# Kernel optimization log

Measured on AMD Instinct MI355X. Metric: run time of the kernel, lower is better.

Reference implementation:

```python
import jax, jax.numpy as jnp
import numpy as np

TEMPERATURE = 0.1
LOSS_SCALE = 1.0
LAMBD = 0.5


def setup_inputs() -> dict:
    key = jax.random.key(0)
    k1, k2 = jax.random.split(key)
    B, D = 4096, 768
    predicted = jax.random.normal(k1, (B, D), dtype=jnp.float32)
    target = jax.random.normal(k2, (B, D), dtype=jnp.float32)
    return {"predicted": predicted, "target": target}


def reference(predicted, target):
    predicted = predicted.astype(jnp.float32)
    target = target.astype(jnp.float32)
    B = predicted.shape[0]

    # Pairwise L2 distances via Gram identity (avoids B x B x D intermediate):
    # ||p_i - t_j||^2 = ||p_i||^2 + ||t_j||^2 - 2 p_i . t_j
    p_sq = jnp.sum(predicted * predicted, axis=-1)  # [B]
    t_sq = jnp.sum(target * target, axis=-1)        # [B]
    cross = predicted @ target.T                    # [B, B]
    sq_dist = p_sq[:, None] + t_sq[None, :] - 2.0 * cross
    distances = jnp.sqrt(jnp.maximum(sq_dist, 0.0))  # [B, B]

    logits = -distances / TEMPERATURE
    # cross-entropy with labels = arange(B): mean of -log_softmax diagonal
    log_probs = jax.nn.log_softmax(logits, axis=-1)
    contrastive_dist_loss = -jnp.mean(jnp.diagonal(log_probs))

    # normalized L1 magnitude loss
    elementwise_l1 = jnp.sum(jnp.abs(predicted - target), axis=-1)  # [B]
    target_magnitude = jnp.sum(jnp.abs(target), axis=-1)            # [B]
    norm_factor = jax.lax.stop_gradient(target_magnitude)
    normalized_magnitude_loss = jnp.mean(elementwise_l1 / norm_factor)

    total_loss = LOSS_SCALE * (
        LAMBD * contrastive_dist_loss + (1.0 - LAMBD) * normalized_magnitude_loss
    )
    return (total_loss, contrastive_dist_loss, normalized_magnitude_loss)
```

## Files before the change

kernel.cpp:

```cpp
#include <hip/hip_runtime.h>
#include <hip/hip_bf16.h>
#include <math.h>

#define B_ROWS 4096
#define D_DIM  768

#define BM 256
#define BN 256
#define BK 32
#define NKT (D_DIM / BK)
#define NBUF 4

typedef __attribute__((ext_vector_type(8))) short bf16x8;
typedef __attribute__((ext_vector_type(4))) float f32x4;

__device__ __forceinline__ unsigned short f32_to_bf16(float x) {
    unsigned int u = __float_as_uint(x);
    return (unsigned short)((u + 0x7fffu + ((u >> 16) & 1u)) >> 16);
}

__device__ __forceinline__ void async_copy16(const unsigned short* g, unsigned short* l) {
    __builtin_amdgcn_global_load_lds(
        (const __attribute__((address_space(1))) unsigned int*)g,
        (__attribute__((address_space(3))) unsigned int*)l,
        16, 0, 0);
}

__global__ void __launch_bounds__(256) rowstats_kernel(
    const float* __restrict__ P, const float* __restrict__ T,
    unsigned short* __restrict__ Pb, unsigned short* __restrict__ Tb,
    float* __restrict__ p_sq, float* __restrict__ t_sq,
    float* __restrict__ diagl, float* __restrict__ magr,
    float* __restrict__ rowsum)
{
    const int wave = threadIdx.x >> 6, lane = threadIdx.x & 63;
    const int i = blockIdx.x * 4 + wave;
    const f32x4* prow = (const f32x4*)(P + (size_t)i * D_DIM);
    const f32x4* trow = (const f32x4*)(T + (size_t)i * D_DIM);
    ushort4* pbrow = (ushort4*)(Pb + (size_t)i * D_DIM);
    ushort4* tbrow = (ushort4*)(Tb + (size_t)i * D_DIM);

    float psq = 0.f, tsq = 0.f, cr = 0.f, l1 = 0.f, tm = 0.f;
    #pragma unroll
    for (int u = 0; u < 3; ++u) {
        const int c4 = u * 64 + lane;
        f32x4 p = prow[c4], t = trow[c4];
        #pragma unroll
        for (int k = 0; k < 4; ++k) {
            psq += p[k] * p[k]; tsq += t[k] * t[k]; cr += p[k] * t[k];
            l1 += fabsf(p[k] - t[k]); tm += fabsf(t[k]);
        }
        pbrow[c4] = make_ushort4(f32_to_bf16(p[0]), f32_to_bf16(p[1]),
                                 f32_to_bf16(p[2]), f32_to_bf16(p[3]));
        tbrow[c4] = make_ushort4(f32_to_bf16(t[0]), f32_to_bf16(t[1]),
                                 f32_to_bf16(t[2]), f32_to_bf16(t[3]));
    }
    #pragma unroll
    for (int m = 1; m < 64; m <<= 1) {
        psq += __shfl_xor(psq, m, 64);
        tsq += __shfl_xor(tsq, m, 64);
        cr  += __shfl_xor(cr,  m, 64);
        l1  += __shfl_xor(l1,  m, 64);
        tm  += __shfl_xor(tm,  m, 64);
    }
    if (lane == 0) {
        p_sq[i] = psq;
        t_sq[i] = tsq;
        float sq = fmaxf(psq + tsq - 2.0f * cr, 0.0f);
        diagl[i] = -sqrtf(sq) * 10.0f;
        magr[i]  = l1 / tm;
        rowsum[i] = 0.0f;
    }
}

__global__ void __launch_bounds__(512, 2) lse_gemm_kernel(
    const unsigned short* __restrict__ Pb, const unsigned short* __restrict__ Tb,
    const float* __restrict__ p_sq, const float* __restrict__ t_sq,
    const float* __restrict__ diagl, float* __restrict__ rowsum)
{
    __shared__ __align__(16) unsigned short S[NBUF][2][BM * BK];

    const int tid  = threadIdx.x;
    const int lane = tid & 63, wave = tid >> 6;

    const int flat = blockIdx.x;
    const int xcd  = flat & 7;
    const int s    = flat >> 3;
    const int ti   = ((xcd >> 1) << 2) + (s >> 3);
    const int tj   = ((xcd & 1) << 3) + (s & 7);
    const int i0   = ti * BM, j0 = tj * BN;

    const int wm = wave >> 2, wn = wave & 3;
    const int row16 = lane & 15, quad = lane >> 4;

    int aoff[8], boff[4];
    #pragma unroll
    for (int mt = 0; mt < 8; ++mt) {
        const int R = wm * 128 + mt * 16 + row16;
        aoff[mt] = R * BK + ((quad ^ ((R >> 1) & 3)) << 3);
    }
    #pragma unroll
    for (int nt = 0; nt < 4; ++nt) {
        const int R = wn * 64 + nt * 16 + row16;
        boff[nt] = R * BK + ((quad ^ ((R >> 1) & 3)) << 3);
    }

    const bool isB = wave >= 4;
    const int  sw  = wave & 3;
    const int  q   = lane & 3;
    const unsigned short* gsrc = isB ? Tb : Pb;
    const int  r0g = isB ? j0 : i0;
    const unsigned short* gp[4];
    int lbase[4];
    #pragma unroll
    for (int j = 0; j < 4; ++j) {
        const int R = sw * 64 + j * 16 + (lane >> 2);
        const int g = q ^ ((R >> 1) & 3);
        gp[j] = gsrc + (size_t)(r0g + R) * D_DIM + g * 8;
        lbase[j] = (sw * 64 + j * 16) * BK;
    }

    f32x4 acc[8][4];
    #pragma unroll
    for (int a = 0; a < 8; ++a)
        #pragma unroll
        for (int b = 0; b < 4; ++b)
            acc[a][b] = (f32x4){0.f, 0.f, 0.f, 0.f};

    auto compute = [&](int buf) {
        const unsigned short* Ab = &S[buf][0][0];
        const unsigned short* Bb = &S[buf][1][0];
        bf16x8 a[8], b[4];
        #pragma unroll
        for (int mt = 0; mt < 8; ++mt) a[mt] = *(const bf16x8*)(Ab + aoff[mt]);
        #pragma unroll
        for (int nt = 0; nt < 4; ++nt) b[nt] = *(const bf16x8*)(Bb + boff[nt]);
        __builtin_amdgcn_s_setprio(1);
        #pragma unroll
        for (int mt = 0; mt < 8; ++mt)
            #pragma unroll
            for (int nt = 0; nt < 4; ++nt)
                acc[mt][nt] = __builtin_amdgcn_mfma_f32_16x16x32_bf16(
                    a[mt], b[nt], acc[mt][nt], 0, 0, 0);
        __builtin_amdgcn_s_setprio(0);
    };

    #pragma unroll
    for (int t = 0; t < 3; ++t)
        #pragma unroll
        for (int j = 0; j < 4; ++j)
            async_copy16(gp[j] + t * BK, &S[t][isB][lbase[j]]);
    asm volatile("s_waitcnt vmcnt(8)" ::: "memory");
    __builtin_amdgcn_s_barrier();

    for (int t = 0; t < NKT - 3; ++t) {
        const int pb = (t + 3) & 3;
        #pragma unroll
        for (int j = 0; j < 4; ++j)
            async_copy16(gp[j] + (t + 3) * BK, &S[pb][isB][lbase[j]]);
        compute(t & 3);
        __builtin_amdgcn_sched_barrier(0);
        asm volatile("s_waitcnt vmcnt(8) lgkmcnt(0)" ::: "memory");
        __builtin_amdgcn_s_barrier();
    }
    compute(21 & 3);
    __builtin_amdgcn_sched_barrier(0);
    asm volatile("s_waitcnt vmcnt(4) lgkmcnt(0)" ::: "memory");
    __builtin_amdgcn_s_barrier();
    compute(22 & 3);
    __builtin_amdgcn_sched_barrier(0);
    asm volatile("s_waitcnt vmcnt(0) lgkmcnt(0)" ::: "memory");
    __builtin_amdgcn_s_barrier();
    compute(23 & 3);

    const float NT_LOG2E = -14.4269504089f;
    const float LOG2E    = 1.44269504089f;
    float tsq_l[4];
    #pragma unroll
    for (int nt = 0; nt < 4; ++nt)
        tsq_l[nt] = t_sq[j0 + wn * 64 + nt * 16 + row16];

    #pragma unroll
    for (int mt = 0; mt < 8; ++mt) {
        #pragma unroll
        for (int r = 0; r < 4; ++r) {
            const int i = i0 + wm * 128 + mt * 16 + quad * 4 + r;
            const float psq = p_sq[i];
            const float c0  = -diagl[i] * LOG2E;
            float sfin = 0.f;
            #pragma unroll
            for (int nt = 0; nt < 4; ++nt) {
                float c  = acc[mt][nt][r];
                float sq = fmaxf(fmaf(-2.0f, c, psq + tsq_l[nt]), 0.0f);
                float d  = sqrtf(sq);
                float y  = fmaf(d, NT_LOG2E, c0);
                sfin += exp2f(y);
            }
            #pragma unroll
            for (int m = 1; m < 16; m <<= 1) sfin += __shfl_xor(sfin, m, 64);
            if (row16 == 0) atomicAdd(&rowsum[i], sfin);
        }
    }
}

__global__ void __launch_bounds__(256) finalize_kernel(
    const float* __restrict__ rowsum, const float* __restrict__ magr,
    float* __restrict__ out)
{
    const int tid = threadIdx.x;
    double sc = 0.0, sm = 0.0;
    for (int i = tid; i < B_ROWS; i += 256) {
        sc += log((double)rowsum[i]);
        sm += (double)magr[i];
    }
    #pragma unroll
    for (int m = 1; m < 64; m <<= 1) {
        sc += __shfl_xor(sc, m, 64);
        sm += __shfl_xor(sm, m, 64);
    }
    __shared__ double red[4][2];
    const int wave = tid >> 6, lane = tid & 63;
    if (lane == 0) { red[wave][0] = sc; red[wave][1] = sm; }
    __syncthreads();
    if (tid == 0) {
        sc = red[0][0] + red[1][0] + red[2][0] + red[3][0];
        sm = red[0][1] + red[1][1] + red[2][1] + red[3][1];
        double lc = sc / (double)B_ROWS;
        double lm = sm / (double)B_ROWS;
        out[0] = (float)(0.5 * lc + 0.5 * lm);
        out[1] = (float)lc;
        out[2] = (float)lm;
    }
}

extern "C" void kernel_launch(void* const* d_in, const int* in_sizes, int n_in,
                              void* d_out, int out_size, void* d_ws, size_t ws_size,
                              hipStream_t stream) {
    const float* P = (const float*)d_in[0];
    const float* T = (const float*)d_in[1];
    float* out = (float*)d_out;

    char* ws = (char*)d_ws;
    float* rowsum = (float*)ws;               ws += B_ROWS * sizeof(float);
    float* p_sq   = (float*)ws;               ws += B_ROWS * sizeof(float);
    float* t_sq   = (float*)ws;               ws += B_ROWS * sizeof(float);
    float* diagl  = (float*)ws;               ws += B_ROWS * sizeof(float);
    float* magr   = (float*)ws;               ws += B_ROWS * sizeof(float);
    unsigned short* Pb = (unsigned short*)ws; ws += (size_t)B_ROWS * D_DIM * 2;
    unsigned short* Tb = (unsigned short*)ws;

    rowstats_kernel<<<B_ROWS / 4, 256, 0, stream>>>(
        P, T, Pb, Tb, p_sq, t_sq, diagl, magr, rowsum);
    lse_gemm_kernel<<<(B_ROWS / BM) * (B_ROWS / BN), 512, 0, stream>>>(
        Pb, Tb, p_sq, t_sq, diagl, rowsum);
    finalize_kernel<<<1, 256, 0, stream>>>(rowsum, magr, out);
}
```

Measured before the change: 126.3 us.

## Pre-tile bf16 operands by K-slice, split MMA into phases, fuse finalize

The row-stats kernel now writes the bf16 copies of P and T in a K-tiled, pre-swizzled layout, so each 32-wide K slice of 256 rows is one contiguous block and the async LDS copies read fully coalesced lines. The GEMM main loop is split into two half-tile phases that interleave LDS reads, global prefetch and MFMA, with barriers between them. The separate finalize kernel is removed: the last GEMM block to finish, found through an atomic ticket counter, performs the final reduction. This saves a kernel launch and improves load efficiency, at the cost of extra barriers per K step and the ticket and fence logic.

Result: slower. 152.5 us (+20.8%).

```diff
diff --git a/kernel.cpp b/kernel.cpp
--- a/kernel.cpp
+++ b/kernel.cpp
@@ -10,6 +10,8 @@
 #define BK 32
 #define NKT (D_DIM / BK)
 #define NBUF 4
+#define KT_STRIDE (B_ROWS * 32)
+#define NBLK ((B_ROWS / BM) * (B_ROWS / BN))
 
 typedef __attribute__((ext_vector_type(8))) short bf16x8;
 typedef __attribute__((ext_vector_type(4))) float f32x4;
@@ -31,14 +33,14 @@
     unsigned short* __restrict__ Pb, unsigned short* __restrict__ Tb,
     float* __restrict__ p_sq, float* __restrict__ t_sq,
     float* __restrict__ diagl, float* __restrict__ magr,
-    float* __restrict__ rowsum)
+    float* __restrict__ rowsum, int* __restrict__ donecnt)
 {
     const int wave = threadIdx.x >> 6, lane = threadIdx.x & 63;
     const int i = blockIdx.x * 4 + wave;
+    if (blockIdx.x == 0 && threadIdx.x == 0) *donecnt = 0;
     const f32x4* prow = (const f32x4*)(P + (size_t)i * D_DIM);
     const f32x4* trow = (const f32x4*)(T + (size_t)i * D_DIM);
-    ushort4* pbrow = (ushort4*)(Pb + (size_t)i * D_DIM);
-    ushort4* tbrow = (ushort4*)(Tb + (size_t)i * D_DIM);
+    const int swz = (i >> 1) & 3;
 
     float psq = 0.f, tsq = 0.f, cr = 0.f, l1 = 0.f, tm = 0.f;
     #pragma unroll
@@ -50,10 +52,15 @@
             psq += p[k] * p[k]; tsq += t[k] * t[k]; cr += p[k] * t[k];
             l1 += fabsf(p[k] - t[k]); tm += fabsf(t[k]);
         }
-        pbrow[c4] = make_ushort4(f32_to_bf16(p[0]), f32_to_bf16(p[1]),
-                                 f32_to_bf16(p[2]), f32_to_bf16(p[3]));
-        tbrow[c4] = make_ushort4(f32_to_bf16(t[0]), f32_to_bf16(t[1]),
-                                 f32_to_bf16(t[2]), f32_to_bf16(t[3]));
+        const int kt  = c4 >> 3;
+        const int cc  = (c4 >> 1) & 3;
+        const int sub = c4 & 1;
+        const size_t doff = (size_t)kt * KT_STRIDE + (size_t)i * 32
+                          + (size_t)(((cc ^ swz) << 3) + (sub << 2));
+        *(ushort4*)(Pb + doff) = make_ushort4(f32_to_bf16(p[0]), f32_to_bf16(p[1]),
+                                              f32_to_bf16(p[2]), f32_to_bf16(p[3]));
+        *(ushort4*)(Tb + doff) = make_ushort4(f32_to_bf16(t[0]), f32_to_bf16(t[1]),
+                                              f32_to_bf16(t[2]), f32_to_bf16(t[3]));
     }
     #pragma unroll
     for (int m = 1; m < 64; m <<= 1) {
@@ -76,9 +83,12 @@
 __global__ void __launch_bounds__(512, 2) lse_gemm_kernel(
     const unsigned short* __restrict__ Pb, const unsigned short* __restrict__ Tb,
     const float* __restrict__ p_sq, const float* __restrict__ t_sq,
-    const float* __restrict__ diagl, float* __restrict__ rowsum)
+    const float* __restrict__ diagl, float* __restrict__ rowsum,
+    const float* __restrict__ magr, int* __restrict__ donecnt,
+    float* __restrict__ out)
 {
     __shared__ __align__(16) unsigned short S[NBUF][2][BM * BK];
+    __shared__ int ticket;
 
     const int tid  = threadIdx.x;
     const int lane = tid & 63, wave = tid >> 6;
@@ -107,17 +117,15 @@
 
     const bool isB = wave >= 4;
     const int  sw  = wave & 3;
-    const int  q   = lane & 3;
     const unsigned short* gsrc = isB ? Tb : Pb;
     const int  r0g = isB ? j0 : i0;
     const unsigned short* gp[4];
-    int lbase[4];
+    int lb[4];
     #pragma unroll
     for (int j = 0; j < 4; ++j) {
-        const int R = sw * 64 + j * 16 + (lane >> 2);
-        const int g = q ^ ((R >> 1) & 3);
-        gp[j] = gsrc + (size_t)(r0g + R) * D_DIM + g * 8;
-        lbase[j] = (sw * 64 + j * 16) * BK;
+        const int rblk = sw * 64 + j * 16;
+        gp[j] = gsrc + (size_t)(r0g + rblk) * 32 + lane * 8;
+        lb[j] = rblk * BK;
     }
 
     f32x4 acc[8][4];
@@ -127,51 +135,73 @@
         for (int b = 0; b < 4; ++b)
             acc[a][b] = (f32x4){0.f, 0.f, 0.f, 0.f};
 
-    auto compute = [&](int buf) {
-        const unsigned short* Ab = &S[buf][0][0];
-        const unsigned short* Bb = &S[buf][1][0];
-        bf16x8 a[8], b[4];
-        #pragma unroll
-        for (int mt = 0; mt < 8; ++mt) a[mt] = *(const bf16x8*)(Ab + aoff[mt]);
+    auto tile_phases = [&](int cb, int pb, size_t koff, bool stg) {
+        const unsigned short* Ab = &S[cb][0][0];
+        const unsigned short* Bb = &S[cb][1][0];
+        bf16x8 a[4], b[4];
+        #pragma unroll
+        for (int mt = 0; mt < 4; ++mt) a[mt] = *(const bf16x8*)(Ab + aoff[mt]);
         #pragma unroll
         for (int nt = 0; nt < 4; ++nt) b[nt] = *(const bf16x8*)(Bb + boff[nt]);
+        if (stg) {
+            async_copy16(gp[0] + koff, &S[pb][isB][lb[0]]);
+            async_copy16(gp[1] + koff, &S[pb][isB][lb[1]]);
+        }
+        __builtin_amdgcn_s_barrier();
+        asm volatile("s_waitcnt lgkmcnt(0)" ::: "memory");
+        __builtin_amdgcn_sched_barrier(0);
         __builtin_amdgcn_s_setprio(1);
         #pragma unroll
-        for (int mt = 0; mt < 8; ++mt)
+        for (int mt = 0; mt < 4; ++mt)
             #pragma unroll
             for (int nt = 0; nt < 4; ++nt)
                 acc[mt][nt] = __builtin_amdgcn_mfma_f32_16x16x32_bf16(
                     a[mt], b[nt], acc[mt][nt], 0, 0, 0);
         __builtin_amdgcn_s_setprio(0);
+        __builtin_amdgcn_s_barrier();
+        bf16x8 a2[4];
+        #pragma unroll
+        for (int mt = 0; mt < 4; ++mt) a2[mt] = *(const bf16x8*)(Ab + aoff[4 + mt]);
+        if (stg) {
+            async_copy16(gp[2] + koff, &S[pb][isB][lb[2]]);
+            async_copy16(gp[3] + koff, &S[pb][isB][lb[3]]);
+        }
+        __builtin_amdgcn_s_barrier();
+        asm volatile("s_waitcnt lgkmcnt(0)" ::: "memory");
+        __builtin_amdgcn_sched_barrier(0);
+        __builtin_amdgcn_s_setprio(1);
+        #pragma unroll
+        for (int mt = 0; mt < 4; ++mt)
+            #pragma unroll
+            for (int nt = 0; nt < 4; ++nt)
+                acc[4 + mt][nt] = __builtin_amdgcn_mfma_f32_16x16x32_bf16(
+                    a2[mt], b[nt], acc[4 + mt][nt], 0, 0, 0);
+        __builtin_amdgcn_s_setprio(0);
     };
 
     #pragma unroll
     for (int t = 0; t < 3; ++t)
         #pragma unroll
         for (int j = 0; j < 4; ++j)
-            async_copy16(gp[j] + t * BK, &S[t][isB][lbase[j]]);
+            async_copy16(gp[j] + (size_t)t * KT_STRIDE, &S[t][isB][lb[j]]);
     asm volatile("s_waitcnt vmcnt(8)" ::: "memory");
     __builtin_amdgcn_s_barrier();
 
     for (int t = 0; t < NKT - 3; ++t) {
-        const int pb = (t + 3) & 3;
-        #pragma unroll
-        for (int j = 0; j < 4; ++j)
-            async_copy16(gp[j] + (t + 3) * BK, &S[pb][isB][lbase[j]]);
-        compute(t & 3);
+        tile_phases(t & 3, (t + 3) & 3, (size_t)(t + 3) * KT_STRIDE, true);
         __builtin_amdgcn_sched_barrier(0);
-        asm volatile("s_waitcnt vmcnt(8) lgkmcnt(0)" ::: "memory");
-        __builtin_amdgcn_s_barrier();
-    }
-    compute(21 & 3);
+        asm volatile("s_waitcnt vmcnt(8)" ::: "memory");
+        __builtin_amdgcn_s_barrier();
+    }
+    tile_phases((NKT - 3) & 3, 0, 0, false);
     __builtin_amdgcn_sched_barrier(0);
-    asm volatile("s_waitcnt vmcnt(4) lgkmcnt(0)" ::: "memory");
+    asm volatile("s_waitcnt vmcnt(4)" ::: "memory");
     __builtin_amdgcn_s_barrier();
-    compute(22 & 3);
+    tile_phases((NKT - 2) & 3, 0, 0, false);
     __builtin_amdgcn_sched_barrier(0);
-    asm volatile("s_waitcnt vmcnt(0) lgkmcnt(0)" ::: "memory");
+    asm volatile("s_waitcnt vmcnt(0)" ::: "memory");
     __builtin_amdgcn_s_barrier();
-    compute(23 & 3);
+    tile_phases((NKT - 1) & 3, 0, 0, false);
 
     const float NT_LOG2E = -14.4269504089f;
     const float LOG2E    = 1.44269504089f;
@@ -201,35 +231,39 @@
             if (row16 == 0) atomicAdd(&rowsum[i], sfin);
         }
     }
-}
-
-__global__ void __launch_bounds__(256) finalize_kernel(
-    const float* __restrict__ rowsum, const float* __restrict__ magr,
-    float* __restrict__ out)
-{
-    const int tid = threadIdx.x;
-    double sc = 0.0, sm = 0.0;
-    for (int i = tid; i < B_ROWS; i += 256) {
-        sc += log((double)rowsum[i]);
-        sm += (double)magr[i];
-    }
-    #pragma unroll
-    for (int m = 1; m < 64; m <<= 1) {
-        sc += __shfl_xor(sc, m, 64);
-        sm += __shfl_xor(sm, m, 64);
-    }
-    __shared__ double red[4][2];
-    const int wave = tid >> 6, lane = tid & 63;
-    if (lane == 0) { red[wave][0] = sc; red[wave][1] = sm; }
+
+    __threadfence();
     __syncthreads();
-    if (tid == 0) {
-        sc = red[0][0] + red[1][0] + red[2][0] + red[3][0];
-        sm = red[0][1] + red[1][1] + red[2][1] + red[3][1];
-        double lc = sc / (double)B_ROWS;
-        double lm = sm / (double)B_ROWS;
-        out[0] = (float)(0.5 * lc + 0.5 * lm);
-        out[1] = (float)lc;
-        out[2] = (float)lm;
+    if (tid == 0) ticket = atomicAdd(donecnt, 1);
+    __syncthreads();
+    if (ticket == NBLK - 1) {
+        __threadfence();
+        double sc = 0.0, sm = 0.0;
+        for (int i = tid; i < B_ROWS; i += 512) {
+            float rs = __hip_atomic_load(&rowsum[i], __ATOMIC_RELAXED,
+                                         __HIP_MEMORY_SCOPE_AGENT);
+            sc += log((double)rs);
+            sm += (double)magr[i];
+        }
+        #pragma unroll
+        for (int m = 1; m < 64; m <<= 1) {
+            sc += __shfl_xor(sc, m, 64);
+            sm += __shfl_xor(sm, m, 64);
+        }
+        double* red = (double*)&S[0][0][0];
+        __syncthreads();
+        if (lane == 0) { red[wave * 2] = sc; red[wave * 2 + 1] = sm; }
+        __syncthreads();
+        if (tid == 0) {
+            sc = 0.0; sm = 0.0;
+            #pragma unroll
+            for (int w2 = 0; w2 < 8; ++w2) { sc += red[w2 * 2]; sm += red[w2 * 2 + 1]; }
+            double lc = sc / (double)B_ROWS;
+            double lm = sm / (double)B_ROWS;
+            out[0] = (float)(0.5 * lc + 0.5 * lm);
+            out[1] = (float)lc;
+            out[2] = (float)lm;
+        }
     }
 }
 
@@ -246,12 +280,12 @@
     float* t_sq   = (float*)ws;               ws += B_ROWS * sizeof(float);
     float* diagl  = (float*)ws;               ws += B_ROWS * sizeof(float);
     float* magr   = (float*)ws;               ws += B_ROWS * sizeof(float);
+    int*   donecnt = (int*)ws;                ws += 16;
     unsigned short* Pb = (unsigned short*)ws; ws += (size_t)B_ROWS * D_DIM * 2;
     unsigned short* Tb = (unsigned short*)ws;
 
     rowstats_kernel<<<B_ROWS / 4, 256, 0, stream>>>(
-        P, T, Pb, Tb, p_sq, t_sq, diagl, magr, rowsum);
-    lse_gemm_kernel<<<(B_ROWS / BM) * (B_ROWS / BN), 512, 0, stream>>>(
-        Pb, Tb, p_sq, t_sq, diagl, rowsum);
-    finalize_kernel<<<1, 256, 0, stream>>>(rowsum, magr, out);
-}
+        P, T, Pb, Tb, p_sq, t_sq, diagl, magr, rowsum, donecnt);
+    lse_gemm_kernel<<<NBLK, 512, 0, stream>>>(
+        Pb, Tb, p_sq, t_sq, diagl, rowsum, magr, donecnt, out);
+}
```
